# Kernel optimization log

Hardware: AMD Instinct MI355X
Metric: run time of the kernel (lower is better)

## Reference

```python
import jax, jax.numpy as jnp
import numpy as np


def setup_inputs() -> dict:
    key = jax.random.key(0)
    k1, k2 = jax.random.split(key)
    B, Lp, Lw, D = 4, 256, 200, 768
    bert_emb = jax.random.normal(k1, (B, Lp, D), dtype=jnp.float32)
    # pieces2word[b, w, p] == 1 iff wordpiece p belongs to word w
    pieces2word = jax.random.randint(k2, (B, Lw, Lp), 0, 2, dtype=jnp.int32)
    return {"bert_emb": bert_emb, "pieces2word": pieces2word}


def reference(bert_emb, pieces2word):
    # Faithful to EmbeddingLayer.forward:
    #   min_value = bert_emb.min().item()  (a detached scalar in torch)
    #   _bert_embs = bert_emb.unsqueeze(1).expand(-1, Lw, -1, -1)
    #   masked_fill where pieces2word == 0 with min_value; max over piece dim
    min_value = jax.lax.stop_gradient(jnp.min(bert_emb))
    # [B, Lw, Lp, D] broadcast, masked, reduced over pieces (axis=2)
    masked = jnp.where(pieces2word[:, :, :, None] != 0,
                       bert_emb[:, None, :, :],
                       min_value)
    word_reps = jnp.max(masked, axis=2)  # [B, Lw, D]
    return word_reps
```

## Files before the change

kernel.cpp:

```cpp
#include <hip/hip_runtime.h>
#include <hip/hip_bf16.h>


#define B_  4
#define LP_ 256
#define LW_ 200
#define D_  768
#define D4_ (D_ / 4)
#define NMIN_BLOCKS 64

__global__ __launch_bounds__(256) void block_min(
    const float4* __restrict__ x, float* __restrict__ ws)
{
    const int n4 = (B_ * LP_ * D_) / 4;
    float m = __uint_as_float(0x7F800000u);
    for (int i = blockIdx.x * blockDim.x + threadIdx.x; i < n4;
         i += gridDim.x * blockDim.x) {
        float4 v = x[i];
        m = fminf(m, fminf(fminf(v.x, v.y), fminf(v.z, v.w)));
    }
    #pragma unroll
    for (int off = 32; off > 0; off >>= 1)
        m = fminf(m, __shfl_down(m, off, 64));
    __shared__ float sm[4];
    int lane = threadIdx.x & 63, wid = threadIdx.x >> 6;
    if (lane == 0) sm[wid] = m;
    __syncthreads();
    if (threadIdx.x == 0) {
        float bm = fminf(fminf(sm[0], sm[1]), fminf(sm[2], sm[3]));
        ws[blockIdx.x] = bm;
    }
}

__device__ __forceinline__ float4 max4(float4 a, float4 b) {
    return make_float4(fmaxf(a.x, b.x), fmaxf(a.y, b.y),
                       fmaxf(a.z, b.z), fmaxf(a.w, b.w));
}

__global__ __launch_bounds__(256) void word_max(
    const float* __restrict__ emb, const int* __restrict__ p2w,
    const float* __restrict__ ws, float* __restrict__ out)
{
    const int bw = blockIdx.x;
    const int b = bw / LW_;
    const int w = bw - b * LW_;
    const int tid = threadIdx.x;
    const int lane = tid & 63, wid = tid >> 6;

    __shared__ int   active[LP_];
    __shared__ int   wcnt[4];
    __shared__ float s_minv;

    if (wid == 0) {
        float m = ws[lane];
        #pragma unroll
        for (int off = 32; off > 0; off >>= 1)
            m = fminf(m, __shfl_down(m, off, 64));
        if (lane == 0) s_minv = m;
    }

    const int* mrow = p2w + (b * LW_ + w) * LP_;
    const bool act = (mrow[tid] != 0);
    const unsigned long long bal = __ballot(act);
    if (lane == 0) wcnt[wid] = __popcll(bal);
    __syncthreads();

    int off = 0;
    #pragma unroll
    for (int i = 0; i < 4; ++i) off += (i < wid) ? wcnt[i] : 0;
    if (act) {
        int pos = off + __popcll(bal & ((1ull << lane) - 1ull));
        active[pos] = tid;
    }
    const int n = wcnt[0] + wcnt[1] + wcnt[2] + wcnt[3];
    __syncthreads();

    if (tid >= D4_) return;

    const float  minv = s_minv;
    const float4* erow = (const float4*)(emb + b * LP_ * D_);
    float4 acc = make_float4(minv, minv, minv, minv);

    int i = 0;
    for (; i + 4 <= n; i += 4) {
        int p0 = active[i + 0];
        int p1 = active[i + 1];
        int p2 = active[i + 2];
        int p3 = active[i + 3];
        float4 v0 = erow[p0 * D4_ + tid];
        float4 v1 = erow[p1 * D4_ + tid];
        float4 v2 = erow[p2 * D4_ + tid];
        float4 v3 = erow[p3 * D4_ + tid];
        acc = max4(acc, max4(max4(v0, v1), max4(v2, v3)));
    }
    for (; i < n; ++i) {
        acc = max4(acc, erow[active[i] * D4_ + tid]);
    }

    ((float4*)out)[(b * LW_ + w) * D4_ + tid] = acc;
}

extern "C" void kernel_launch(void* const* d_in, const int* in_sizes, int n_in,
                              void* d_out, int out_size, void* d_ws, size_t ws_size,
                              hipStream_t stream) {
    const float* emb = (const float*)d_in[0];
    const int*   p2w = (const int*)d_in[1];
    float*       out = (float*)d_out;
    float*       ws  = (float*)d_ws;

    block_min<<<NMIN_BLOCKS, 256, 0, stream>>>((const float4*)emb, ws);
    word_max<<<B_ * LW_, 256, 0, stream>>>(emb, p2w, ws, out);
}
```

Baseline: 77.21 us.

## Drop global min kernel, compute min only for empty words; split D across waves

Removes the separate global-min reduction kernel. The max of the active pieces is used directly, and the global minimum is computed only when a word has no active pieces, since min_value can only reach the output in that case. Each (batch, word) is now split into three single-wave blocks covering 64 float4 columns each, which removes the idle waves and block barriers. The trade-off is that the mask row is read and compacted three times per word, and an empty word falls back to a slow single-wave scan of the whole tensor.

Result: faster. 72.17 us (-6.5%).

```diff
diff --git a/kernel.cpp b/kernel.cpp
--- a/kernel.cpp
+++ b/kernel.cpp
@@ -1,5 +1,4 @@
 #include <hip/hip_runtime.h>
-#include <hip/hip_bf16.h>
 
 
 #define B_  4
@@ -7,97 +6,75 @@
 #define LW_ 200
 #define D_  768
 #define D4_ (D_ / 4)
-#define NMIN_BLOCKS 64
-
-__global__ __launch_bounds__(256) void block_min(
-    const float4* __restrict__ x, float* __restrict__ ws)
-{
-    const int n4 = (B_ * LP_ * D_) / 4;
-    float m = __uint_as_float(0x7F800000u);
-    for (int i = blockIdx.x * blockDim.x + threadIdx.x; i < n4;
-         i += gridDim.x * blockDim.x) {
-        float4 v = x[i];
-        m = fminf(m, fminf(fminf(v.x, v.y), fminf(v.z, v.w)));
-    }
-    #pragma unroll
-    for (int off = 32; off > 0; off >>= 1)
-        m = fminf(m, __shfl_down(m, off, 64));
-    __shared__ float sm[4];
-    int lane = threadIdx.x & 63, wid = threadIdx.x >> 6;
-    if (lane == 0) sm[wid] = m;
-    __syncthreads();
-    if (threadIdx.x == 0) {
-        float bm = fminf(fminf(sm[0], sm[1]), fminf(sm[2], sm[3]));
-        ws[blockIdx.x] = bm;
-    }
-}
+#define CHUNKS 3
+#define NBLK (B_ * LW_ * CHUNKS)
 
 __device__ __forceinline__ float4 max4(float4 a, float4 b) {
     return make_float4(fmaxf(a.x, b.x), fmaxf(a.y, b.y),
                        fmaxf(a.z, b.z), fmaxf(a.w, b.w));
 }
 
-__global__ __launch_bounds__(256) void word_max(
+__global__ __launch_bounds__(64) void word_max(
     const float* __restrict__ emb, const int* __restrict__ p2w,
-    const float* __restrict__ ws, float* __restrict__ out)
+    float* __restrict__ out)
 {
-    const int bw = blockIdx.x;
-    const int b = bw / LW_;
-    const int w = bw - b * LW_;
-    const int tid = threadIdx.x;
-    const int lane = tid & 63, wid = tid >> 6;
+    const int blk   = blockIdx.x;
+    const int chunk = blk % CHUNKS;
+    const int bw    = blk / CHUNKS;
+    const int b     = bw / LW_;
+    const int w     = bw - b * LW_;
+    const int lane  = threadIdx.x;
 
-    __shared__ int   active[LP_];
-    __shared__ int   wcnt[4];
-    __shared__ float s_minv;
+    __shared__ int active[LP_];
+    const int* mrow = p2w + (b * LW_ + w) * LP_;
+    int cnt = 0;
+    #pragma unroll
+    for (int r = 0; r < 4; ++r) {
+        const bool a = (mrow[r * 64 + lane] != 0);
+        const unsigned long long bal = __ballot(a);
+        if (a) {
+            int pos = cnt + __popcll(bal & ((1ull << lane) - 1ull));
+            active[pos] = r * 64 + lane;
+        }
+        cnt += __popcll(bal);
+    }
 
-    if (wid == 0) {
-        float m = ws[lane];
+    const float4* erow = (const float4*)(emb + b * LP_ * D_) + chunk * 64 + lane;
+    float4*       orow = (float4*)out + bw * D4_ + chunk * 64 + lane;
+
+    if (cnt == 0) {
+        const float4* x = (const float4*)emb;
+        const int n4 = (B_ * LP_ * D_) / 4;
+        float m = __uint_as_float(0x7F800000u);
+        for (int i = lane; i < n4; i += 64) {
+            float4 v = x[i];
+            m = fminf(m, fminf(fminf(v.x, v.y), fminf(v.z, v.w)));
+        }
         #pragma unroll
         for (int off = 32; off > 0; off >>= 1)
             m = fminf(m, __shfl_down(m, off, 64));
-        if (lane == 0) s_minv = m;
+        m = __shfl(m, 0, 64);
+        *orow = make_float4(m, m, m, m);
+        return;
     }
 
-    const int* mrow = p2w + (b * LW_ + w) * LP_;
-    const bool act = (mrow[tid] != 0);
-    const unsigned long long bal = __ballot(act);
-    if (lane == 0) wcnt[wid] = __popcll(bal);
-    __syncthreads();
-
-    int off = 0;
-    #pragma unroll
-    for (int i = 0; i < 4; ++i) off += (i < wid) ? wcnt[i] : 0;
-    if (act) {
-        int pos = off + __popcll(bal & ((1ull << lane) - 1ull));
-        active[pos] = tid;
-    }
-    const int n = wcnt[0] + wcnt[1] + wcnt[2] + wcnt[3];
-    __syncthreads();
-
-    if (tid >= D4_) return;
-
-    const float  minv = s_minv;
-    const float4* erow = (const float4*)(emb + b * LP_ * D_);
-    float4 acc = make_float4(minv, minv, minv, minv);
-
-    int i = 0;
-    for (; i + 4 <= n; i += 4) {
-        int p0 = active[i + 0];
-        int p1 = active[i + 1];
-        int p2 = active[i + 2];
-        int p3 = active[i + 3];
-        float4 v0 = erow[p0 * D4_ + tid];
-        float4 v1 = erow[p1 * D4_ + tid];
-        float4 v2 = erow[p2 * D4_ + tid];
-        float4 v3 = erow[p3 * D4_ + tid];
+    float4 acc = erow[active[0] * D4_];
+    int i = 1;
+    for (; i + 4 <= cnt; i += 4) {
+        const int p0 = active[i + 0];
+        const int p1 = active[i + 1];
+        const int p2 = active[i + 2];
+        const int p3 = active[i + 3];
+        const float4 v0 = erow[p0 * D4_];
+        const float4 v1 = erow[p1 * D4_];
+        const float4 v2 = erow[p2 * D4_];
+        const float4 v3 = erow[p3 * D4_];
         acc = max4(acc, max4(max4(v0, v1), max4(v2, v3)));
     }
-    for (; i < n; ++i) {
-        acc = max4(acc, erow[active[i] * D4_ + tid]);
-    }
+    for (; i < cnt; ++i)
+        acc = max4(acc, erow[active[i] * D4_]);
 
-    ((float4*)out)[(b * LW_ + w) * D4_ + tid] = acc;
+    *orow = acc;
 }
 
 extern "C" void kernel_launch(void* const* d_in, const int* in_sizes, int n_in,
@@ -106,8 +83,7 @@
     const float* emb = (const float*)d_in[0];
     const int*   p2w = (const int*)d_in[1];
     float*       out = (float*)d_out;
-    float*       ws  = (float*)d_ws;
+    (void)d_ws; (void)ws_size;
 
-    block_min<<<NMIN_BLOCKS, 256, 0, stream>>>((const float4*)emb, ws);
-    word_max<<<B_ * LW_, 256, 0, stream>>>(emb, p2w, ws, out);
+    word_max<<<NBLK, 64, 0, stream>>>(emb, p2w, out);
 }
```
